# Kernel optimization log

Hardware: AMD Instinct MI355X
Metric: run time of the kernel (lower is better)

Reference implementation:

```python
import jax, jax.numpy as jnp
import numpy as np

N = 100000          # nodes
E = 1600000         # edges
D_IN = 128
HID = 256
N_CLASSES = 10
N_GRAPHS = 64


def gcn_conv(x, src, dst, W, b, n_nodes):
    """PyG GCNConv: add self-loops, symmetric deg^{-1/2} normalization, x@W, scatter-add."""
    h = x @ W  # [N, out]
    loop = jnp.arange(n_nodes, dtype=src.dtype)
    src2 = jnp.concatenate([src, loop])
    dst2 = jnp.concatenate([dst, loop])
    deg = jax.ops.segment_sum(jnp.ones(src2.shape[0], x.dtype), dst2, num_segments=n_nodes)
    dinv = jax.lax.rsqrt(deg)  # deg >= 1 thanks to self-loops
    norm = dinv[src2] * dinv[dst2]  # [E+N]
    msg = norm[:, None] * h[src2]   # [E+N, out]
    return jax.ops.segment_sum(msg, dst2, num_segments=n_nodes) + b


def setup_inputs() -> dict:
    key = jax.random.key(0)
    ks = jax.random.split(key, 12)
    x = jax.random.normal(ks[0], (N, D_IN), dtype=jnp.float32)
    edge_index = jax.random.randint(ks[1], (2, E), 0, N, dtype=jnp.int64)
    batch = jnp.sort(jax.random.randint(ks[2], (N,), 0, N_GRAPHS, dtype=jnp.int64))
    def glorot(k, shape):
        lim = float(np.sqrt(6.0 / (shape[0] + shape[1])))
        return jax.random.uniform(k, shape, jnp.float32, -lim, lim)
    W1 = glorot(ks[3], (D_IN, HID));  b1 = jnp.zeros((HID,), jnp.float32)
    W2 = glorot(ks[4], (HID, HID));   b2 = jnp.zeros((HID,), jnp.float32)
    Wf1 = glorot(ks[5], (HID, HID));  bf1 = jnp.zeros((HID,), jnp.float32)
    Wf2 = glorot(ks[6], (HID, N_CLASSES)); bf2 = jnp.zeros((N_CLASSES,), jnp.float32)
    return {"x": x, "edge_index": edge_index, "batch": batch,
            "W1": W1, "b1": b1, "W2": W2, "b2": b2,
            "Wf1": Wf1, "bf1": bf1, "Wf2": Wf2, "bf2": bf2}


def reference(x, edge_index, batch, W1, b1, W2, b2, Wf1, bf1, Wf2, bf2):
    src, dst = edge_index[0], edge_index[1]
    h = jax.nn.relu(gcn_conv(x, src, dst, W1, b1, N))
    h = jax.nn.relu(gcn_conv(h, src, dst, W2, b2, N))
    # global mean pool over graph ids
    summed = jax.ops.segment_sum(h, batch, num_segments=N_GRAPHS)  # [G, HID]
    counts = jax.ops.segment_sum(jnp.ones((N,), h.dtype), batch, num_segments=N_GRAPHS)
    pooled = summed / jnp.maximum(counts, 1.0)[:, None]
    z = jax.nn.relu(pooled @ Wf1 + bf1)
    alpha = jax.nn.softplus(z @ Wf2 + bf2) + 0.001
    return alpha
```

## Files before the change

kernel.cpp:

```cpp
#include <hip/hip_runtime.h>
#include <math.h>

#define NN   100000
#define NE   1600000
#define DIN  128
#define HID  256
#define NG   64
#define NCLS 10

#define NBLK 128
#define EPB  (NE / NBLK)
#define NBUK 512
#define NPB  196
#define NHIST (NBUK * NBLK)
#define NBR  ((NN + 127) / 128)

using bf16x8 = __attribute__((ext_vector_type(8))) short;
using f32x4  = __attribute__((ext_vector_type(4))) float;
using f32x2  = __attribute__((ext_vector_type(2))) float;
using u32x2  = __attribute__((ext_vector_type(2))) unsigned int;
using u32x4  = __attribute__((ext_vector_type(4))) unsigned int;

static __device__ __forceinline__ unsigned short f2bf(float f) {
    unsigned u = __float_as_uint(f);
    u += 0x7fff + ((u >> 16) & 1);
    return (unsigned short)(u >> 16);
}

static __device__ __forceinline__ unsigned char f32_to_fp8(float f) {
    float a = fminf(fabsf(f), 448.f);
    unsigned bits = __float_as_uint(a * 0x1p-120f);
    bits += 0x7ffff + ((bits >> 20) & 1);
    unsigned e4 = (bits >> 20) & 0x7f;
    return (unsigned char)(e4 | (f < 0.f ? 0x80u : 0u));
}
#if __has_builtin(__builtin_amdgcn_cvt_pk_f32_fp8)
#define HAVE_CVT_FP8 1
#endif
static __device__ __forceinline__ void fp8x4_to_f32(unsigned u, float* f) {
#ifdef HAVE_CVT_FP8
    f32x2 lo = __builtin_amdgcn_cvt_pk_f32_fp8((int)u, false);
    f32x2 hi = __builtin_amdgcn_cvt_pk_f32_fp8((int)u, true);
    f[0] = lo[0]; f[1] = lo[1]; f[2] = hi[0]; f[3] = hi[1];
#else
#pragma unroll
    for (int k = 0; k < 4; ++k) {
        unsigned b = (u >> (8 * k)) & 0xffu;
        unsigned bits = ((b & 0x80u) << 24) | ((b & 0x7fu) << 20);
        f[k] = __uint_as_float(bits) * 0x1p+120f;
    }
#endif
}
static __device__ __forceinline__ int4 fp8x8_to_bf16x8(unsigned lo, unsigned hi) {
    float f[8];
    fp8x4_to_f32(lo, f);
    fp8x4_to_f32(hi, f + 4);
    int4 r;
    r.x = (int)((__float_as_uint(f[0]) >> 16) | (__float_as_uint(f[1]) & 0xffff0000u));
    r.y = (int)((__float_as_uint(f[2]) >> 16) | (__float_as_uint(f[3]) & 0xffff0000u));
    r.z = (int)((__float_as_uint(f[4]) >> 16) | (__float_as_uint(f[5]) & 0xffff0000u));
    r.w = (int)((__float_as_uint(f[6]) >> 16) | (__float_as_uint(f[7]) & 0xffff0000u));
    return r;
}


__global__ __launch_bounds__(256) void k_hist(const int* __restrict__ dst,
                                              int* __restrict__ histg) {
    __shared__ int h[NBUK];
    const int t = threadIdx.x;
    for (int i = t; i < NBUK; i += 256) h[i] = 0;
    __syncthreads();
    const int e0 = blockIdx.x * EPB, e1 = e0 + EPB;
    for (int e = e0 + t; e < e1; e += 256)
        atomicAdd(&h[(unsigned)__builtin_nontemporal_load(&dst[e]) / NPB], 1);
    __syncthreads();
    for (int i = t; i < NBUK; i += 256)
        histg[i * NBLK + blockIdx.x] = h[i];
}

__global__ __launch_bounds__(256) void k_bsum2(const int* __restrict__ d,
                                               int* __restrict__ bsum) {
    __shared__ int sd[256];
    int t = threadIdx.x;
    const int4 v = *(const int4*)&d[blockIdx.x * 1024 + t * 4];
    sd[t] = v.x + v.y + v.z + v.w;
    __syncthreads();
    for (int off = 128; off > 0; off >>= 1) {
        if (t < off) sd[t] += sd[t + off];
        __syncthreads();
    }
    if (t == 0) bsum[blockIdx.x] = sd[0];
}

__global__ void k_scanb2(const int* __restrict__ bsum, int* __restrict__ boff,
                         const int* __restrict__ batch, float* __restrict__ countsf) {
    __shared__ int tmp[64];
    int t = threadIdx.x;
    int v = bsum[t];
    tmp[t] = v; __syncthreads();
    for (int off = 1; off < 64; off <<= 1) {
        int u = (t >= off) ? tmp[t - off] : 0;
        __syncthreads();
        tmp[t] += u;
        __syncthreads();
    }
    boff[t] = tmp[t] - v;
    int g = t;
    int lo = 0, hi = NN;
    while (lo < hi) { int mid = (lo + hi) >> 1; if (batch[mid] < g) lo = mid + 1; else hi = mid; }
    int lb = lo;
    lo = 0; hi = NN;
    while (lo < hi) { int mid = (lo + hi) >> 1; if (batch[mid] <= g) lo = mid + 1; else hi = mid; }
    countsf[g] = (float)(lo - lb);
}

__global__ __launch_bounds__(256) void k_offs2(int* __restrict__ d,
                                               const int* __restrict__ boff) {
    __shared__ int ts[256];
    int t = threadIdx.x;
    int base = blockIdx.x * 1024 + t * 4;
    int4 v = *(const int4*)&d[base];
    int s = v.x + v.y + v.z + v.w;
    ts[t] = s; __syncthreads();
    for (int off = 1; off < 256; off <<= 1) {
        int u = (t >= off) ? ts[t - off] : 0;
        __syncthreads();
        ts[t] += u;
        __syncthreads();
    }
    int run = ts[t] - s + boff[blockIdx.x];
    int4 o;
    o.x = run; run += v.x;
    o.y = run; run += v.y;
    o.z = run; run += v.z;
    o.w = run; run += v.w;
    *(int4*)&d[base] = o;
}

__global__ __launch_bounds__(256) void k_scatter(const int* __restrict__ src,
                                                 const int* __restrict__ dst,
                                                 const int* __restrict__ offg,
                                                 unsigned* __restrict__ pairs) {
    __shared__ int cur[NBUK];
    const int t = threadIdx.x;
    for (int i = t; i < NBUK; i += 256) cur[i] = offg[i * NBLK + blockIdx.x];
    __syncthreads();
    const int e0 = blockIdx.x * EPB, e1 = e0 + EPB;
    for (int e = e0 + t; e < e1; e += 256) {
        int d = __builtin_nontemporal_load(&dst[e]);
        int sv = __builtin_nontemporal_load(&src[e]);
        int b = (unsigned)d / NPB;
        int li = d - b * NPB;
        unsigned pk = ((unsigned)li << 24) | (unsigned)sv;
        int p = atomicAdd(&cur[b], 1);
        __builtin_nontemporal_store(pk, &pairs[p]);
    }
}

__global__ __launch_bounds__(256) void k_csr(const unsigned* __restrict__ pairs,
                                             const int* __restrict__ offg,
                                             int* __restrict__ csr,
                                             int* __restrict__ deg,
                                             float* __restrict__ dinv,
                                             int* __restrict__ offs) {
    __shared__ int cnt[NPB];
    __shared__ int loff[256];
    __shared__ int cur[NPB];
    const int b = blockIdx.x, t = threadIdx.x;
    const int s     = offg[b * NBLK];
    const int e_end = (b == NBUK - 1) ? NE : offg[(b + 1) * NBLK];
    const int nb0   = b * NPB;
    const int nnod  = min(NPB, NN - nb0);
    if (t < NPB) cnt[t] = 0;
    __syncthreads();
    for (int e = s + t; e < e_end; e += 256)
        atomicAdd(&cnt[pairs[e] >> 24], 1);
    __syncthreads();
    int v = (t < NPB) ? cnt[t] : 0;
    loff[t] = v;
    __syncthreads();
    for (int off = 1; off < 256; off <<= 1) {
        int u = (t >= off) ? loff[t - off] : 0;
        __syncthreads();
        loff[t] += u;
        __syncthreads();
    }
    int myoff = loff[t] - v;
    __syncthreads();
    loff[t] = myoff;
    if (t < NPB) cur[t] = 0;
    __syncthreads();
    if (t < nnod) {
        int node = nb0 + t;
        int dg = cnt[t];
        deg[node]  = dg;
        dinv[node] = rsqrtf((float)(dg + 1));
        offs[node] = s + myoff;
    }
    for (int e = s + t; e < e_end; e += 256) {
        unsigned pk = pairs[e];
        int li = pk >> 24;
        int p = atomicAdd(&cur[li], 1);
        csr[s + loff[li] + p] = (int)(pk & 0xffffffu);
    }
}


#define XQ (NN * 32)

__global__ void k_cast_all(const float* __restrict__ x, const float* __restrict__ dinv,
                           unsigned char* __restrict__ xs8,
                           const float* __restrict__ W1, unsigned short* __restrict__ Wt1,
                           const float* __restrict__ W2, unsigned short* __restrict__ Wt2) {
    int i = blockIdx.x * blockDim.x + threadIdx.x;
    if (i < XQ) {
        int nd = i >> 5;
        int q  = i & 31;
        float dv = dinv[nd];
        const float4 v = *(const float4*)&x[(size_t)nd * DIN + q * 4];
        uchar4 o;
        o.x = f32_to_fp8(v.x * dv); o.y = f32_to_fp8(v.y * dv);
        o.z = f32_to_fp8(v.z * dv); o.w = f32_to_fp8(v.w * dv);
        *(uchar4*)&xs8[(size_t)nd * DIN + q * 4] = o;
        return;
    }
    int j = i - XQ;
    if (j < DIN * HID) {
        int k = j >> 8, nc = j & 255;
        Wt1[nc * DIN + k] = f2bf(W1[j]);
    } else if (j < (DIN + HID) * HID) {
        int jj = j - DIN * HID;
        int k = jj >> 8, nc = jj & 255;
        Wt2[nc * HID + k] = f2bf(W2[jj]);
    }
}


template <int MODE>
__global__ __launch_bounds__(512) void k_gemm_mfma(const unsigned char* __restrict__ A8,
                                                   const unsigned short* __restrict__ Wt,
                                                   const float* __restrict__ dinv,
                                                   const float* __restrict__ bias,
                                                   void* __restrict__ outp,
                                                   const int* __restrict__ batch,
                                                   int M, int K) {
    __shared__ unsigned short As[128 * 72];
    __shared__ unsigned short Bs[256 * 72];
    __shared__ float psum[4][256];
    __shared__ int gloc[128];
    const int t = threadIdx.x;
    const int lane = t & 63;
    const int wid = t >> 6;
    const int wr = wid & 1, wc = wid >> 1;
    const int bm = blockIdx.x * 128;
    const int lr = lane & 15;
    const int ko = (lane >> 4) << 3;

    f32x4 acc[4][4] = {};

    const int arow = t >> 2;
    const int akq  = (t & 3) << 4;
    const int brow = t >> 1;
    const int bkq  = (t & 1) << 5;

    int g0 = 0, gend = 0;
    if (MODE == 2) {
        g0 = batch[bm];
        gend = batch[min(bm + 127, M - 1)];
        for (int i = t; i < 4 * 256; i += 512) ((float*)psum)[i] = 0.f;
        if (t < 128) gloc[t] = (bm + t < M) ? min(batch[bm + t] - g0, 3) : 0;
    }

    for (int kk = 0; kk < K; kk += 64) {
        {
            int row = bm + arow;
            u32x4 v; v.x = v.y = v.z = v.w = 0u;
            if (row < M) v = *(const u32x4*)&A8[(size_t)row * K + kk + akq];
            *(int4*)&As[arow * 72 + akq]     = fp8x8_to_bf16x8(v.x, v.y);
            *(int4*)&As[arow * 72 + akq + 8] = fp8x8_to_bf16x8(v.z, v.w);
        }
        {
            const unsigned short* wsrc = &Wt[(size_t)brow * K + kk + bkq];
#pragma unroll
            for (int q = 0; q < 4; ++q)
                *(int4*)&Bs[brow * 72 + bkq + q * 8] = *(const int4*)&wsrc[q * 8];
        }
        __syncthreads();
#pragma unroll
        for (int ks = 0; ks < 64; ks += 32) {
            bf16x8 af[4], bfr[4];
#pragma unroll
            for (int mf = 0; mf < 4; ++mf)
                af[mf] = *(const bf16x8*)&As[(wr * 64 + mf * 16 + lr) * 72 + ks + ko];
#pragma unroll
            for (int nf = 0; nf < 4; ++nf)
                bfr[nf] = *(const bf16x8*)&Bs[(wc * 64 + nf * 16 + lr) * 72 + ks + ko];
#pragma unroll
            for (int mf = 0; mf < 4; ++mf)
#pragma unroll
                for (int nf = 0; nf < 4; ++nf)
                    acc[mf][nf] = __builtin_amdgcn_mfma_f32_16x16x32_bf16(af[mf], bfr[nf], acc[mf][nf], 0, 0, 0);
        }
        __syncthreads();
    }

    if (MODE == 1) {
        unsigned char* out8 = (unsigned char*)outp;
#pragma unroll
        for (int mf = 0; mf < 4; ++mf) {
#pragma unroll
            for (int b = 0; b < 4; ++b) {
                int row = bm + wr * 64 + mf * 16 + (lane >> 4) * 4 + b;
                if (row >= M) continue;
                float dv = dinv[row];
#pragma unroll
                for (int nf = 0; nf < 4; ++nf) {
                    int col = wc * 64 + nf * 16 + lr;
                    float v = fmaxf(acc[mf][nf][b] + bias[col], 0.f);
                    out8[(size_t)row * HID + col] = f32_to_fp8(dv * v);
                }
            }
        }
    } else {
        const int q4 = (lane >> 4) << 2;
        if (gend == g0) {
#pragma unroll
            for (int nf = 0; nf < 4; ++nf) {
                const int lcol = wc * 64 + nf * 16 + lr;
                const float bb = bias[lcol];
                float rsum = 0.f;
#pragma unroll
                for (int mf = 0; mf < 4; ++mf)
#pragma unroll
                    for (int b = 0; b < 4; ++b) {
                        int lrow = wr * 64 + mf * 16 + q4 + b;
                        if (bm + lrow < M) rsum += fmaxf(acc[mf][nf][b] + bb, 0.f);
                    }
                rsum += __shfl_xor(rsum, 16);
                rsum += __shfl_xor(rsum, 32);
                if ((lane >> 4) == 0) atomicAdd(&psum[0][lcol], rsum);
            }
        } else {
#pragma unroll
            for (int nf = 0; nf < 4; ++nf) {
                const int lcol = wc * 64 + nf * 16 + lr;
                const float bb = bias[lcol];
                float run = 0.f; int gcur = 0;
#pragma unroll
                for (int mf = 0; mf < 4; ++mf) {
#pragma unroll
                    for (int b = 0; b < 4; ++b) {
                        int lrow = wr * 64 + mf * 16 + q4 + b;
                        if (bm + lrow < M) {
                            int gl = gloc[lrow];
                            float v = fmaxf(acc[mf][nf][b] + bb, 0.f);
                            if (gl != gcur) {
                                if (run != 0.f) atomicAdd(&psum[gcur][lcol], run);
                                run = 0.f; gcur = gl;
                            }
                            run += v;
                        }
                    }
                }
                if (run != 0.f) atomicAdd(&psum[gcur][lcol], run);
            }
        }
        __syncthreads();
        float* scratch = (float*)outp;
        size_t base = (size_t)blockIdx.x * 1024;
        for (int i = t; i < 1024; i += 512)
            __builtin_nontemporal_store(((const float*)psum)[i], &scratch[base + i]);
    }
}


__global__ __launch_bounds__(128) void k_reduce(const float* __restrict__ scratch,
                                                const int* __restrict__ batch,
                                                float* __restrict__ pooled) {
    const int g = blockIdx.x >> 1, by = blockIdx.x & 1;
    const int t = threadIdx.x;
    const int col = by * 128 + t;
    int lo = 0, hi = NN;
    while (lo < hi) { int mid = (lo + hi) >> 1; if (batch[mid] < g) lo = mid + 1; else hi = mid; }
    int s = lo;
    lo = s; hi = NN;
    while (lo < hi) { int mid = (lo + hi) >> 1; if (batch[mid] <= g) lo = mid + 1; else hi = mid; }
    int e = lo;
    float sum = 0.f;
    if (e > s) {
        int bx0 = s >> 7, bx1 = (e - 1) >> 7;
        for (int bx = bx0; bx <= bx1; ++bx) {
            int gl = min(g - batch[bx << 7], 3);
            sum += scratch[(size_t)bx * 1024 + gl * 256 + col];
        }
    }
    pooled[g * HID + col] = sum;
}


__global__ __launch_bounds__(256) void k_agg256(const unsigned char* __restrict__ hs,
                                                const int* __restrict__ csr,
                                                const int* __restrict__ offs,
                                                const int* __restrict__ deg,
                                                const float* __restrict__ dinv,
                                                unsigned char* __restrict__ out, int n) {
    int wid = threadIdx.x >> 6, lane = threadIdx.x & 63;
    int node = blockIdx.x * 4 + wid;
    if (node >= n) return;
    int c = lane << 2;
    float a0, a1, a2, a3;
    {
        unsigned u = *(const unsigned*)&hs[(size_t)node * HID + c];
        float f[4]; fp8x4_to_f32(u, f);
        a0 = f[0]; a1 = f[1]; a2 = f[2]; a3 = f[3];
    }
    int s0 = offs[node], cnt = deg[node];
    for (int base = 0; base < cnt; base += 64) {
        int nb = min(64, cnt - base);
        int idx = (lane < nb) ? __builtin_nontemporal_load(&csr[s0 + base + lane]) : 0;
        int i = 0;
        for (; i + 8 <= nb; i += 8) {
            unsigned v[8];
#pragma unroll
            for (int k = 0; k < 8; ++k) {
                int j = __shfl(idx, i + k);
                v[k] = *(const unsigned*)&hs[(size_t)j * HID + c];
            }
#pragma unroll
            for (int k = 0; k < 8; ++k) {
                float f[4]; fp8x4_to_f32(v[k], f);
                a0 += f[0]; a1 += f[1]; a2 += f[2]; a3 += f[3];
            }
        }
        for (; i + 4 <= nb; i += 4) {
            unsigned v[4];
#pragma unroll
            for (int k = 0; k < 4; ++k) {
                int j = __shfl(idx, i + k);
                v[k] = *(const unsigned*)&hs[(size_t)j * HID + c];
            }
#pragma unroll
            for (int k = 0; k < 4; ++k) {
                float f[4]; fp8x4_to_f32(v[k], f);
                a0 += f[0]; a1 += f[1]; a2 += f[2]; a3 += f[3];
            }
        }
        for (; i < nb; ++i) {
            int j = __shfl(idx, i);
            unsigned u = *(const unsigned*)&hs[(size_t)j * HID + c];
            float f[4]; fp8x4_to_f32(u, f);
            a0 += f[0]; a1 += f[1]; a2 += f[2]; a3 += f[3];
        }
    }
    float dv = dinv[node];
    uchar4 r;
    r.x = f32_to_fp8(dv * a0); r.y = f32_to_fp8(dv * a1);
    r.z = f32_to_fp8(dv * a2); r.w = f32_to_fp8(dv * a3);
    *(uchar4*)&out[(size_t)node * HID + c] = r;
}


__global__ __launch_bounds__(256) void k_agg128(const unsigned char* __restrict__ xs,
                                                const int* __restrict__ csr,
                                                const int* __restrict__ offs,
                                                const int* __restrict__ deg,
                                                const float* __restrict__ dinv,
                                                unsigned char* __restrict__ out, int n) {
    int wid = threadIdx.x >> 6, lane = threadIdx.x & 63;
    int node = blockIdx.x * 4 + wid;
    if (node >= n) return;
    int half = lane >> 5, l32 = lane & 31;
    int c = l32 << 2;
    float a0 = 0.f, a1 = 0.f, a2 = 0.f, a3 = 0.f;
    if (half == 0) {
        unsigned u = *(const unsigned*)&xs[(size_t)node * DIN + c];
        float f[4]; fp8x4_to_f32(u, f);
        a0 = f[0]; a1 = f[1]; a2 = f[2]; a3 = f[3];
    }
    int s0 = offs[node], cnt = deg[node];
    for (int base = 0; base < cnt; base += 64) {
        int nb = min(64, cnt - base);
        int idx = (lane < nb) ? __builtin_nontemporal_load(&csr[s0 + base + lane]) : 0;
        int i = 0;
        for (; i + 8 <= nb; i += 8) {
            unsigned v[4];
#pragma unroll
            for (int k = 0; k < 4; ++k) {
                int j = __shfl(idx, i + 2 * k + half);
                v[k] = *(const unsigned*)&xs[(size_t)j * DIN + c];
            }
#pragma unroll
            for (int k = 0; k < 4; ++k) {
                float f[4]; fp8x4_to_f32(v[k], f);
                a0 += f[0]; a1 += f[1]; a2 += f[2]; a3 += f[3];
            }
        }
        for (; i < nb; i += 2) {
            int e = i + half;
            int j = __shfl(idx, e < nb ? e : 0);
            if (e < nb) {
                unsigned u = *(const unsigned*)&xs[(size_t)j * DIN + c];
                float f[4]; fp8x4_to_f32(u, f);
                a0 += f[0]; a1 += f[1]; a2 += f[2]; a3 += f[3];
            }
        }
    }
    a0 += __shfl_xor(a0, 32);
    a1 += __shfl_xor(a1, 32);
    a2 += __shfl_xor(a2, 32);
    a3 += __shfl_xor(a3, 32);
    if (half == 0) {
        float dv = dinv[node];
        uchar4 r;
        r.x = f32_to_fp8(dv * a0); r.y = f32_to_fp8(dv * a1);
        r.z = f32_to_fp8(dv * a2); r.w = f32_to_fp8(dv * a3);
        *(uchar4*)&out[(size_t)node * DIN + c] = r;
    }
}


__global__ __launch_bounds__(256) void k_mlp(const float* __restrict__ pooled,
                                             const float* __restrict__ countsf,
                                             const float* __restrict__ Wf1,
                                             const float* __restrict__ bf1,
                                             const float* __restrict__ Wf2,
                                             const float* __restrict__ bf2,
                                             float* __restrict__ out) {
    __shared__ float p[HID];
    __shared__ float z[HID];
    int g = blockIdx.x, t = threadIdx.x;
    float cnt = fmaxf(countsf[g], 1.0f);
    p[t] = pooled[g * HID + t] / cnt;
    __syncthreads();
    float accz = bf1[t];
    for (int k = 0; k < HID; ++k)
        accz = fmaf(p[k], Wf1[k * HID + t], accz);
    z[t] = fmaxf(accz, 0.f);
    __syncthreads();
    if (t < NCLS) {
        float o = bf2[t];
        for (int k = 0; k < HID; ++k)
            o = fmaf(z[k], Wf2[k * NCLS + t], o);
        float sp = fmaxf(o, 0.f) + log1pf(expf(-fabsf(o)));
        out[g * NCLS + t] = sp + 0.001f;
    }
}


extern "C" void kernel_launch(void* const* d_in, const int* in_sizes, int n_in,
                              void* d_out, int out_size, void* d_ws, size_t ws_size,
                              hipStream_t stream) {
    const float* x     = (const float*)d_in[0];
    const int*   ei    = (const int*)d_in[1];
    const int*   batch = (const int*)d_in[2];
    const float* W1    = (const float*)d_in[3];
    const float* b1    = (const float*)d_in[4];
    const float* W2    = (const float*)d_in[5];
    const float* b2    = (const float*)d_in[6];
    const float* Wf1   = (const float*)d_in[7];
    const float* bf1   = (const float*)d_in[8];
    const float* Wf2   = (const float*)d_in[9];
    const float* bf2   = (const float*)d_in[10];
    float* out = (float*)d_out;

    const int* srcv = ei;
    const int* dstv = ei + NE;

    char* p = (char*)d_ws;
    auto take = [&](size_t bytes) -> char* {
        char* q = p; p += (bytes + 255) & ~(size_t)255; return q;
    };
    char* big0 = take((size_t)NN * HID * 2);
    char* big1 = take((size_t)NN * HID * 2);
    unsigned char*  xs8 = (unsigned char*)big0;
    unsigned char*  xa8 = (unsigned char*)(big0 + (size_t)NN * DIN);
    unsigned char*  h8  = (unsigned char*)big1;
    unsigned char*  r8  = (unsigned char*)big0;
    float* scratch = (float*)(big1 + (size_t)NN * HID);
    unsigned* pairs = (unsigned*)big1;
    unsigned short* wt1  = (unsigned short*)take((size_t)DIN * HID * 2);
    unsigned short* wt2  = (unsigned short*)take((size_t)HID * HID * 2);
    int*   histg   = (int*)take((size_t)NHIST * 4);
    int*   bsum    = (int*)take(64 * 4);
    int*   boff    = (int*)take(64 * 4);
    int*   deg     = (int*)take((size_t)NN * 4);
    int*   offs    = (int*)take((size_t)NN * 4);
    int*   csr     = (int*)take((size_t)NE * 4);
    float* dinv    = (float*)take((size_t)NN * 4);
    float* pooled  = (float*)take((size_t)NG * HID * 4);
    float* countsf = (float*)take((size_t)NG * 4);

    k_hist<<<NBLK, 256, 0, stream>>>(dstv, histg);
    k_bsum2<<<64, 256, 0, stream>>>(histg, bsum);
    k_scanb2<<<1, 64, 0, stream>>>(bsum, boff, batch, countsf);
    k_offs2<<<64, 256, 0, stream>>>(histg, boff);
    k_scatter<<<NBLK, 256, 0, stream>>>(srcv, dstv, histg, pairs);
    k_csr<<<NBUK, 256, 0, stream>>>(pairs, histg, csr, deg, dinv, offs);

    int cast_total = XQ + (DIN + HID) * HID;
    k_cast_all<<<(cast_total + 255) / 256, 256, 0, stream>>>(x, dinv, xs8, W1, wt1, W2, wt2);

    k_agg128<<<(NN + 3) / 4, 256, 0, stream>>>(xs8, csr, offs, deg, dinv, xa8, NN);
    k_gemm_mfma<1><<<NBR, 512, 0, stream>>>(xa8, wt1, dinv, b1, (void*)h8, batch, NN, DIN);
    k_agg256<<<(NN + 3) / 4, 256, 0, stream>>>(h8, csr, offs, deg, dinv, r8, NN);
    k_gemm_mfma<2><<<NBR, 512, 0, stream>>>(r8, wt2, dinv, b2, (void*)scratch, batch, NN, HID);
    k_reduce<<<2 * NG, 128, 0, stream>>>(scratch, batch, pooled);

    k_mlp<<<NG, 256, 0, stream>>>(pooled, countsf, Wf1, bf1, Wf2, bf2, out);
}
```

Baseline: 327.9 us.

## Fuse layer-2 aggregation into the GEMM and fold pooling reduce into MLP

The second-layer neighbour aggregation now writes its per-node sums as bf16 straight into shared memory, and the same block runs the MFMA GEMM with W2 on them, using 64-row tiles. This removes the fp8 round trip of the aggregated features through global memory and one kernel launch. The separate reduce kernel is also folded into the MLP kernel, removing another launch. In exchange the tiles are smaller, the 8 waves of each block do the gather before any MFMA work, and the larger shared-memory footprint may reduce occupancy.

```diff
diff --git a/kernel.cpp b/kernel.cpp
--- a/kernel.cpp
+++ b/kernel.cpp
@@ -14,6 +14,7 @@
 #define NPB  196
 #define NHIST (NBUK * NBLK)
 #define NBR  ((NN + 127) / 128)
+#define NBR2 ((NN + 63) / 64)
 
 using bf16x8 = __attribute__((ext_vector_type(8))) short;
 using f32x4  = __attribute__((ext_vector_type(4))) float;
@@ -236,18 +237,14 @@
 }
 
 
-template <int MODE>
-__global__ __launch_bounds__(512) void k_gemm_mfma(const unsigned char* __restrict__ A8,
-                                                   const unsigned short* __restrict__ Wt,
-                                                   const float* __restrict__ dinv,
-                                                   const float* __restrict__ bias,
-                                                   void* __restrict__ outp,
-                                                   const int* __restrict__ batch,
-                                                   int M, int K) {
+__global__ __launch_bounds__(512) void k_gemm1(const unsigned char* __restrict__ A8,
+                                               const unsigned short* __restrict__ Wt,
+                                               const float* __restrict__ dinv,
+                                               const float* __restrict__ bias,
+                                               unsigned char* __restrict__ out8,
+                                               int M, int K) {
     __shared__ unsigned short As[128 * 72];
     __shared__ unsigned short Bs[256 * 72];
-    __shared__ float psum[4][256];
-    __shared__ int gloc[128];
     const int t = threadIdx.x;
     const int lane = t & 63;
     const int wid = t >> 6;
@@ -263,14 +260,6 @@
     const int brow = t >> 1;
     const int bkq  = (t & 1) << 5;
 
-    int g0 = 0, gend = 0;
-    if (MODE == 2) {
-        g0 = batch[bm];
-        gend = batch[min(bm + 127, M - 1)];
-        for (int i = t; i < 4 * 256; i += 512) ((float*)psum)[i] = 0.f;
-        if (t < 128) gloc[t] = (bm + t < M) ? min(batch[bm + t] - g0, 3) : 0;
-    }
-
     for (int kk = 0; kk < K; kk += 64) {
         {
             int row = bm + arow;
@@ -304,159 +293,168 @@
         __syncthreads();
     }
 
-    if (MODE == 1) {
-        unsigned char* out8 = (unsigned char*)outp;
-#pragma unroll
-        for (int mf = 0; mf < 4; ++mf) {
-#pragma unroll
-            for (int b = 0; b < 4; ++b) {
-                int row = bm + wr * 64 + mf * 16 + (lane >> 4) * 4 + b;
-                if (row >= M) continue;
-                float dv = dinv[row];
-#pragma unroll
-                for (int nf = 0; nf < 4; ++nf) {
-                    int col = wc * 64 + nf * 16 + lr;
-                    float v = fmaxf(acc[mf][nf][b] + bias[col], 0.f);
-                    out8[(size_t)row * HID + col] = f32_to_fp8(dv * v);
+#pragma unroll
+    for (int mf = 0; mf < 4; ++mf) {
+#pragma unroll
+        for (int b = 0; b < 4; ++b) {
+            int row = bm + wr * 64 + mf * 16 + (lane >> 4) * 4 + b;
+            if (row >= M) continue;
+            float dv = dinv[row];
+#pragma unroll
+            for (int nf = 0; nf < 4; ++nf) {
+                int col = wc * 64 + nf * 16 + lr;
+                float v = fmaxf(acc[mf][nf][b] + bias[col], 0.f);
+                out8[(size_t)row * HID + col] = f32_to_fp8(dv * v);
+            }
+        }
+    }
+}
+
+
+__global__ __launch_bounds__(512) void k_agg_gemm2(const unsigned char* __restrict__ h8,
+                                                   const int* __restrict__ csr,
+                                                   const int* __restrict__ offs,
+                                                   const int* __restrict__ deg,
+                                                   const float* __restrict__ dinv,
+                                                   const unsigned short* __restrict__ Wt,
+                                                   const float* __restrict__ bias,
+                                                   float* __restrict__ scratch,
+                                                   const int* __restrict__ batch,
+                                                   int M) {
+    __shared__ unsigned short As[64 * 264];
+    __shared__ unsigned short Bs[256 * 72];
+    __shared__ float psum[4][256];
+    __shared__ int gloc[64];
+    const int t = threadIdx.x;
+    const int lane = t & 63;
+    const int wv = t >> 6;
+    const int bm = blockIdx.x * 64;
+    const int lr = lane & 15;
+    const int ko = (lane >> 4) << 3;
+
+    const int g0 = batch[bm];
+    const int gend = batch[min(bm + 63, M - 1)];
+    for (int i = t; i < 4 * 256; i += 512) ((float*)psum)[i] = 0.f;
+    if (t < 64) gloc[t] = (bm + t < M) ? min(batch[bm + t] - g0, 3) : 0;
+
+    const int c = lane << 2;
+    for (int ni = wv; ni < 64; ni += 8) {
+        int node = bm + ni;
+        float a0 = 0.f, a1 = 0.f, a2 = 0.f, a3 = 0.f;
+        if (node < M) {
+            unsigned u = *(const unsigned*)&h8[(size_t)node * HID + c];
+            float f[4]; fp8x4_to_f32(u, f);
+            a0 = f[0]; a1 = f[1]; a2 = f[2]; a3 = f[3];
+            int s0 = offs[node], cnt = deg[node];
+            for (int base = 0; base < cnt; base += 64) {
+                int nb = min(64, cnt - base);
+                int idx = (lane < nb) ? __builtin_nontemporal_load(&csr[s0 + base + lane]) : 0;
+                int i = 0;
+                for (; i + 8 <= nb; i += 8) {
+                    unsigned v[8];
+#pragma unroll
+                    for (int k = 0; k < 8; ++k) {
+                        int j = __shfl(idx, i + k);
+                        v[k] = *(const unsigned*)&h8[(size_t)j * HID + c];
+                    }
+#pragma unroll
+                    for (int k = 0; k < 8; ++k) {
+                        float f2[4]; fp8x4_to_f32(v[k], f2);
+                        a0 += f2[0]; a1 += f2[1]; a2 += f2[2]; a3 += f2[3];
+                    }
+                }
+                for (; i < nb; ++i) {
+                    int j = __shfl(idx, i);
+                    unsigned uu = *(const unsigned*)&h8[(size_t)j * HID + c];
+                    float f2[4]; fp8x4_to_f32(uu, f2);
+                    a0 += f2[0]; a1 += f2[1]; a2 += f2[2]; a3 += f2[3];
                 }
             }
+            float dv = dinv[node];
+            a0 *= dv; a1 *= dv; a2 *= dv; a3 *= dv;
+        }
+        ushort4 w;
+        w.x = f2bf(a0); w.y = f2bf(a1); w.z = f2bf(a2); w.w = f2bf(a3);
+        *(ushort4*)&As[ni * 264 + c] = w;
+    }
+    __syncthreads();
+
+    const int wr = wv & 1, wc = wv >> 1;
+    f32x4 acc[2][4] = {};
+    const int brow = t >> 1;
+    const int bkq  = (t & 1) << 5;
+
+    for (int kk = 0; kk < HID; kk += 64) {
+        const unsigned short* wsrc = &Wt[(size_t)brow * HID + kk + bkq];
+#pragma unroll
+        for (int q = 0; q < 4; ++q)
+            *(int4*)&Bs[brow * 72 + bkq + q * 8] = *(const int4*)&wsrc[q * 8];
+        __syncthreads();
+#pragma unroll
+        for (int ks = 0; ks < 64; ks += 32) {
+            bf16x8 af[2], bfr[4];
+#pragma unroll
+            for (int mf = 0; mf < 2; ++mf)
+                af[mf] = *(const bf16x8*)&As[(wr * 32 + mf * 16 + lr) * 264 + kk + ks + ko];
+#pragma unroll
+            for (int nf = 0; nf < 4; ++nf)
+                bfr[nf] = *(const bf16x8*)&Bs[(wc * 64 + nf * 16 + lr) * 72 + ks + ko];
+#pragma unroll
+            for (int mf = 0; mf < 2; ++mf)
+#pragma unroll
+                for (int nf = 0; nf < 4; ++nf)
+                    acc[mf][nf] = __builtin_amdgcn_mfma_f32_16x16x32_bf16(af[mf], bfr[nf], acc[mf][nf], 0, 0, 0);
+        }
+        __syncthreads();
+    }
+
+    const int q4 = (lane >> 4) << 2;
+    if (gend == g0) {
+#pragma unroll
+        for (int nf = 0; nf < 4; ++nf) {
+            const int lcol = wc * 64 + nf * 16 + lr;
+            const float bb = bias[lcol];
+            float rsum = 0.f;
+#pragma unroll
+            for (int mf = 0; mf < 2; ++mf)
+#pragma unroll
+                for (int b = 0; b < 4; ++b) {
+                    int lrow = wr * 32 + mf * 16 + q4 + b;
+                    if (bm + lrow < M) rsum += fmaxf(acc[mf][nf][b] + bb, 0.f);
+                }
+            rsum += __shfl_xor(rsum, 16);
+            rsum += __shfl_xor(rsum, 32);
+            if ((lane >> 4) == 0) atomicAdd(&psum[0][lcol], rsum);
         }
     } else {
-        const int q4 = (lane >> 4) << 2;
-        if (gend == g0) {
-#pragma unroll
-            for (int nf = 0; nf < 4; ++nf) {
-                const int lcol = wc * 64 + nf * 16 + lr;
-                const float bb = bias[lcol];
-                float rsum = 0.f;
-#pragma unroll
-                for (int mf = 0; mf < 4; ++mf)
-#pragma unroll
-                    for (int b = 0; b < 4; ++b) {
-                        int lrow = wr * 64 + mf * 16 + q4 + b;
-                        if (bm + lrow < M) rsum += fmaxf(acc[mf][nf][b] + bb, 0.f);
-                    }
-                rsum += __shfl_xor(rsum, 16);
-                rsum += __shfl_xor(rsum, 32);
-                if ((lane >> 4) == 0) atomicAdd(&psum[0][lcol], rsum);
-            }
-        } else {
-#pragma unroll
-            for (int nf = 0; nf < 4; ++nf) {
-                const int lcol = wc * 64 + nf * 16 + lr;
-                const float bb = bias[lcol];
-                float run = 0.f; int gcur = 0;
-#pragma unroll
-                for (int mf = 0; mf < 4; ++mf) {
-#pragma unroll
-                    for (int b = 0; b < 4; ++b) {
-                        int lrow = wr * 64 + mf * 16 + q4 + b;
-                        if (bm + lrow < M) {
-                            int gl = gloc[lrow];
-                            float v = fmaxf(acc[mf][nf][b] + bb, 0.f);
-                            if (gl != gcur) {
-                                if (run != 0.f) atomicAdd(&psum[gcur][lcol], run);
-                                run = 0.f; gcur = gl;
-                            }
-                            run += v;
+#pragma unroll
+        for (int nf = 0; nf < 4; ++nf) {
+            const int lcol = wc * 64 + nf * 16 + lr;
+            const float bb = bias[lcol];
+            float run = 0.f; int gcur = 0;
+#pragma unroll
+            for (int mf = 0; mf < 2; ++mf) {
+#pragma unroll
+                for (int b = 0; b < 4; ++b) {
+                    int lrow = wr * 32 + mf * 16 + q4 + b;
+                    if (bm + lrow < M) {
+                        int gl = gloc[lrow];
+                        float v = fmaxf(acc[mf][nf][b] + bb, 0.f);
+                        if (gl != gcur) {
+                            if (run != 0.f) atomicAdd(&psum[gcur][lcol], run);
+                            run = 0.f; gcur = gl;
                         }
+                        run += v;
                     }
                 }
-                if (run != 0.f) atomicAdd(&psum[gcur][lcol], run);
             }
-        }
-        __syncthreads();
-        float* scratch = (float*)outp;
-        size_t base = (size_t)blockIdx.x * 1024;
-        for (int i = t; i < 1024; i += 512)
-            __builtin_nontemporal_store(((const float*)psum)[i], &scratch[base + i]);
-    }
-}
-
-
-__global__ __launch_bounds__(128) void k_reduce(const float* __restrict__ scratch,
-                                                const int* __restrict__ batch,
-                                                float* __restrict__ pooled) {
-    const int g = blockIdx.x >> 1, by = blockIdx.x & 1;
-    const int t = threadIdx.x;
-    const int col = by * 128 + t;
-    int lo = 0, hi = NN;
-    while (lo < hi) { int mid = (lo + hi) >> 1; if (batch[mid] < g) lo = mid + 1; else hi = mid; }
-    int s = lo;
-    lo = s; hi = NN;
-    while (lo < hi) { int mid = (lo + hi) >> 1; if (batch[mid] <= g) lo = mid + 1; else hi = mid; }
-    int e = lo;
-    float sum = 0.f;
-    if (e > s) {
-        int bx0 = s >> 7, bx1 = (e - 1) >> 7;
-        for (int bx = bx0; bx <= bx1; ++bx) {
-            int gl = min(g - batch[bx << 7], 3);
-            sum += scratch[(size_t)bx * 1024 + gl * 256 + col];
-        }
-    }
-    pooled[g * HID + col] = sum;
-}
-
-
-__global__ __launch_bounds__(256) void k_agg256(const unsigned char* __restrict__ hs,
-                                                const int* __restrict__ csr,
-                                                const int* __restrict__ offs,
-                                                const int* __restrict__ deg,
-                                                const float* __restrict__ dinv,
-                                                unsigned char* __restrict__ out, int n) {
-    int wid = threadIdx.x >> 6, lane = threadIdx.x & 63;
-    int node = blockIdx.x * 4 + wid;
-    if (node >= n) return;
-    int c = lane << 2;
-    float a0, a1, a2, a3;
-    {
-        unsigned u = *(const unsigned*)&hs[(size_t)node * HID + c];
-        float f[4]; fp8x4_to_f32(u, f);
-        a0 = f[0]; a1 = f[1]; a2 = f[2]; a3 = f[3];
-    }
-    int s0 = offs[node], cnt = deg[node];
-    for (int base = 0; base < cnt; base += 64) {
-        int nb = min(64, cnt - base);
-        int idx = (lane < nb) ? __builtin_nontemporal_load(&csr[s0 + base + lane]) : 0;
-        int i = 0;
-        for (; i + 8 <= nb; i += 8) {
-            unsigned v[8];
-#pragma unroll
-            for (int k = 0; k < 8; ++k) {
-                int j = __shfl(idx, i + k);
-                v[k] = *(const unsigned*)&hs[(size_t)j * HID + c];
-            }
-#pragma unroll
-            for (int k = 0; k < 8; ++k) {
-                float f[4]; fp8x4_to_f32(v[k], f);
-                a0 += f[0]; a1 += f[1]; a2 += f[2]; a3 += f[3];
-            }
-        }
-        for (; i + 4 <= nb; i += 4) {
-            unsigned v[4];
-#pragma unroll
-            for (int k = 0; k < 4; ++k) {
-                int j = __shfl(idx, i + k);
-                v[k] = *(const unsigned*)&hs[(size_t)j * HID + c];
-            }
-#pragma unroll
-            for (int k = 0; k < 4; ++k) {
-                float f[4]; fp8x4_to_f32(v[k], f);
-                a0 += f[0]; a1 += f[1]; a2 += f[2]; a3 += f[3];
-            }
-        }
-        for (; i < nb; ++i) {
-            int j = __shfl(idx, i);
-            unsigned u = *(const unsigned*)&hs[(size_t)j * HID + c];
-            float f[4]; fp8x4_to_f32(u, f);
-            a0 += f[0]; a1 += f[1]; a2 += f[2]; a3 += f[3];
-        }
-    }
-    float dv = dinv[node];
-    uchar4 r;
-    r.x = f32_to_fp8(dv * a0); r.y = f32_to_fp8(dv * a1);
-    r.z = f32_to_fp8(dv * a2); r.w = f32_to_fp8(dv * a3);
-    *(uchar4*)&out[(size_t)node * HID + c] = r;
+            if (run != 0.f) atomicAdd(&psum[gcur][lcol], run);
+        }
+    }
+    __syncthreads();
+    size_t base = (size_t)blockIdx.x * 1024;
+    for (int i = t; i < 1024; i += 512)
+        __builtin_nontemporal_store(((const float*)psum)[i], &scratch[base + i]);
 }
 
 
@@ -519,7 +517,8 @@
 }
 
 
-__global__ __launch_bounds__(256) void k_mlp(const float* __restrict__ pooled,
+__global__ __launch_bounds__(256) void k_mlp(const float* __restrict__ scratch,
+                                             const int* __restrict__ batch,
                                              const float* __restrict__ countsf,
                                              const float* __restrict__ Wf1,
                                              const float* __restrict__ bf1,
@@ -529,8 +528,22 @@
     __shared__ float p[HID];
     __shared__ float z[HID];
     int g = blockIdx.x, t = threadIdx.x;
+    int lo = 0, hi = NN;
+    while (lo < hi) { int mid = (lo + hi) >> 1; if (batch[mid] < g) lo = mid + 1; else hi = mid; }
+    int s = lo;
+    lo = s; hi = NN;
+    while (lo < hi) { int mid = (lo + hi) >> 1; if (batch[mid] <= g) lo = mid + 1; else hi = mid; }
+    int e = lo;
+    float sum = 0.f;
+    if (e > s) {
+        int bx0 = s >> 6, bx1 = (e - 1) >> 6;
+        for (int bx = bx0; bx <= bx1; ++bx) {
+            int gl = min(g - batch[bx << 6], 3);
+            sum += scratch[(size_t)bx * 1024 + gl * 256 + t];
+        }
+    }
     float cnt = fmaxf(countsf[g], 1.0f);
-    p[t] = pooled[g * HID + t] / cnt;
+    p[t] = sum / cnt;
     __syncthreads();
     float accz = bf1[t];
     for (int k = 0; k < HID; ++k)
@@ -575,7 +588,6 @@
     unsigned char*  xs8 = (unsigned char*)big0;
     unsigned char*  xa8 = (unsigned char*)(big0 + (size_t)NN * DIN);
     unsigned char*  h8  = (unsigned char*)big1;
-    unsigned char*  r8  = (unsigned char*)big0;
     float* scratch = (float*)(big1 + (size_t)NN * HID);
     unsigned* pairs = (unsigned*)big1;
     unsigned short* wt1  = (unsigned short*)take((size_t)DIN * HID * 2);
@@ -587,7 +599,6 @@
     int*   offs    = (int*)take((size_t)NN * 4);
     int*   csr     = (int*)take((size_t)NE * 4);
     float* dinv    = (float*)take((size_t)NN * 4);
-    float* pooled  = (float*)take((size_t)NG * HID * 4);
     float* countsf = (float*)take((size_t)NG * 4);
 
     k_hist<<<NBLK, 256, 0, stream>>>(dstv, histg);
@@ -601,10 +612,8 @@
     k_cast_all<<<(cast_total + 255) / 256, 256, 0, stream>>>(x, dinv, xs8, W1, wt1, W2, wt2);
 
     k_agg128<<<(NN + 3) / 4, 256, 0, stream>>>(xs8, csr, offs, deg, dinv, xa8, NN);
-    k_gemm_mfma<1><<<NBR, 512, 0, stream>>>(xa8, wt1, dinv, b1, (void*)h8, batch, NN, DIN);
-    k_agg256<<<(NN + 3) / 4, 256, 0, stream>>>(h8, csr, offs, deg, dinv, r8, NN);
-    k_gemm_mfma<2><<<NBR, 512, 0, stream>>>(r8, wt2, dinv, b2, (void*)scratch, batch, NN, HID);
-    k_reduce<<<2 * NG, 128, 0, stream>>>(scratch, batch, pooled);
-
-    k_mlp<<<NG, 256, 0, stream>>>(pooled, countsf, Wf1, bf1, Wf2, bf2, out);
-}
+    k_gemm1<<<NBR, 512, 0, stream>>>(xa8, wt1, dinv, b1, h8, NN, DIN);
+    k_agg_gemm2<<<NBR2, 512, 0, stream>>>(h8, csr, offs, deg, dinv, wt2, b2,
+                                          scratch, batch, NN);
+    k_mlp<<<NG, 256, 0, stream>>>(scratch, batch, countsf, Wf1, bf1, Wf2, bf2, out);
+}
```

Measured after the change: 387.7 us (median of 2 runs). 1.18x slower.
